# Kernel tuning notes

Measured on AMD Instinct MI355X. Metric: run time of the kernel, lower is better.

## Reference

```python
import jax, jax.numpy as jnp
import numpy as np

B, N, K, D, H, FF, L, NH = 8, 50, 20, 3, 128, 2048, 3, 8
S = N * K
HD = H // NH


def setup_inputs() -> dict:
    key = jax.random.key(0)
    ks = jax.random.split(key, 16)
    visited = jax.random.uniform(ks[0], (B, S)) < 0.05
    # the single most-recent action per batch row (status flips 0 -> 1)
    action_idx = jax.random.randint(ks[1], (B,), 0, S)
    visited = visited.at[jnp.arange(B), action_idx].set(True)
    feats = jax.random.normal(ks[2], (B, S, D - 1)) * visited[:, :, None]
    state = jnp.concatenate([feats, visited[:, :, None].astype(jnp.float32)], axis=-1)
    prev_state = state.at[jnp.arange(B), action_idx, :].set(0.0)

    def w(k, shape, s=0.02):
        return jax.random.normal(k, shape, dtype=jnp.float32) * s

    return dict(
        prev_state=prev_state, state=state,
        W_pre=w(ks[3], (D, H)), b_pre=jnp.zeros(H),
        Wq=w(ks[4], (L, H, H)), bq=jnp.zeros((L, H)),
        Wk=w(ks[5], (L, H, H)), bk=jnp.zeros((L, H)),
        Wv=w(ks[6], (L, H, H)), bv=jnp.zeros((L, H)),
        Wo=w(ks[7], (L, H, H)), bo=jnp.zeros((L, H)),
        ln1_g=jnp.ones((L, H)), ln1_b=jnp.zeros((L, H)),
        Wff1=w(ks[8], (L, H, FF)), bff1=jnp.zeros((L, FF)),
        Wff2=w(ks[9], (L, FF, H)), bff2=jnp.zeros((L, H)),
        ln2_g=jnp.ones((L, H)), ln2_b=jnp.zeros((L, H)),
        W_comb=w(ks[10], (2 * H, H)), b_comb=jnp.zeros(H),
        W_dec=w(ks[11], (H, H)), b_dec=jnp.zeros(H),
        W_lin=w(ks[12], (S, S)), b_lin=jnp.zeros(S),
    )


def _layer_norm(x, g, b, eps=1e-5):
    m = jnp.mean(x, -1, keepdims=True)
    v = jnp.mean(jnp.square(x - m), -1, keepdims=True)
    return (x - m) * jax.lax.rsqrt(v + eps) * g + b


def _update_mask(state):
    # vectorized equivalent of the original Python-loop scatter mask
    status = state[:, :, -1] != 0                      # visited [B, S], S = K*N channel-major
    mask = status
    vis_kn = status.reshape(B, K, N)
    user_any = vis_kn.any(axis=1)                      # [B, N]: user visited on any channel
    mask = mask | jnp.broadcast_to(user_any[:, None, :], (B, K, N)).reshape(B, S)
    assigned = state.reshape(B, K, N, D).sum(-1) != 0  # [B, K, N]
    full = assigned.sum(-1) >= 2                       # [B, K]: channel already has 2 users
    mask = mask | jnp.broadcast_to(full[:, :, None], (B, K, N)).reshape(B, S)
    return mask


def reference(prev_state, state, W_pre, b_pre, Wq, bq, Wk, bk, Wv, bv, Wo, bo,
              ln1_g, ln1_b, Wff1, bff1, Wff2, bff2, ln2_g, ln2_b,
              W_comb, b_comb, W_dec, b_dec, W_lin, b_lin):
    mask = _update_mask(state)
    # exactly one status change per batch row (sequential RL step)
    diff = prev_state[:, :, -1] != state[:, :, -1]
    act_idx = jnp.argmax(diff, axis=1)                 # [B]

    x = state @ W_pre + b_pre                          # [B, S, H]
    scale = np.float32(1.0 / np.sqrt(HD))
    for i in range(L):  # 3 post-LN transformer encoder layers
        q = (x @ Wq[i] + bq[i]).reshape(B, S, NH, HD)
        k = (x @ Wk[i] + bk[i]).reshape(B, S, NH, HD)
        v = (x @ Wv[i] + bv[i]).reshape(B, S, NH, HD)
        att = jax.nn.softmax(jnp.einsum('bqhd,bkhd->bhqk', q, k) * scale, axis=-1)
        o = jnp.einsum('bhqk,bkhd->bqhd', att, v).reshape(B, S, H) @ Wo[i] + bo[i]
        x = _layer_norm(x + o, ln1_g[i], ln1_b[i])
        ff = jax.nn.relu(x @ Wff1[i] + bff1[i]) @ Wff2[i] + bff2[i]
        x = _layer_norm(x + ff, ln2_g[i], ln2_b[i])

    last = x[jnp.arange(B), act_idx]                   # [B, H]
    combined = jnp.concatenate([x.mean(axis=1), last], axis=-1)  # [B, 2H]
    g = combined @ W_comb + b_comb                     # [B, H]
    dec = x @ W_dec + b_dec                            # [B, S, H]
    scores = jnp.einsum('bsh,bh->bs', dec, g)          # [B, S]
    masked = scores @ W_lin + b_lin                    # Q-Learning head
    return jnp.where(mask, -jnp.inf, masked)
```

## Files before the change

### kernel.cpp

```cpp
#include <hip/hip_runtime.h>
#include <math.h>

#define Bb 8
#define Ss 1000
#define Kk 20
#define Nn 50
#define Dd 3
#define Hh 128
#define FFf 2048
#define Ll 3
#define NHh 8
#define HDd 16
#define ROWS (Bb*Ss)

#define SENTINEL -3.0e38f

typedef unsigned short ush;
typedef short short8 __attribute__((ext_vector_type(8)));
typedef short short4v __attribute__((ext_vector_type(4)));
typedef float f32x4 __attribute__((ext_vector_type(4)));

__device__ __forceinline__ ush f2b(float f) {
  unsigned x = __float_as_uint(f);
  return (ush)((x + 0x7fff + ((x >> 16) & 1)) >> 16);
}

__global__ __launch_bounds__(256) void mask_kernel(const float* __restrict__ state,
                                                   const float* __restrict__ prev_state,
                                                   int* __restrict__ mask, int* __restrict__ act_idx) {
  int b = blockIdx.x, tid = threadIdx.x;
  __shared__ unsigned char status[Ss], assigned[Ss], uany[Nn], fullk[Kk];
  __shared__ int act;
  if (tid == 0) act = 1 << 30;
  __syncthreads();
  for (int s = tid; s < Ss; s += 256) {
    const float* st = state + ((size_t)b * Ss + s) * Dd;
    float f2 = st[2];
    status[s] = (f2 != 0.f);
    assigned[s] = ((st[0] + st[1] + f2) != 0.f);
    float p2 = prev_state[((size_t)b * Ss + s) * Dd + 2];
    if (p2 != f2) atomicMin(&act, s);
  }
  __syncthreads();
  if (tid < Nn) {
    unsigned char a = 0;
    for (int k = 0; k < Kk; ++k) a |= status[k * Nn + tid];
    uany[tid] = a;
  } else if (tid >= 64 && tid < 64 + Kk) {
    int k = tid - 64, cnt = 0;
    for (int n = 0; n < Nn; ++n) cnt += assigned[k * Nn + n];
    fullk[k] = (cnt >= 2);
  }
  __syncthreads();
  for (int s = tid; s < Ss; s += 256)
    mask[b * Ss + s] = (int)(status[s] | uany[s % Nn] | fullk[s / Nn]);
  if (tid == 0) act_idx[b] = (act >= Ss) ? 0 : act;
}

__global__ __launch_bounds__(256) void pre_kernel(const float* __restrict__ state,
                                                  const float* __restrict__ W_pre,
                                                  const float* __restrict__ b_pre,
                                                  float* __restrict__ x, ush* __restrict__ xbf,
                                                  float* __restrict__ mpart) {
  int idx = blockIdx.x * 256 + threadIdx.x;
  if (idx >= ROWS * Hh) return;
  if (idx < Bb * Hh) mpart[idx] = 0.f;
  int row = idx >> 7, n = idx & 127;
  const float* st = state + (size_t)row * Dd;
  float v = b_pre[n] + st[0] * W_pre[n] + st[1] * W_pre[Hh + n] + st[2] * W_pre[2 * Hh + n];
  x[idx] = v;
  xbf[idx] = f2b(v);
}

#define TQKV 144
#define TWO  48
#define TFF1 768
#define TFF2 768
#define TWD  16
#define TBIAS 5
#define TTOT (TQKV+TWO+TFF1+TFF2+TWD+TBIAS)
__global__ __launch_bounds__(256) void transpose_prep(
    const float* __restrict__ Wq, const float* __restrict__ Wk, const float* __restrict__ Wv,
    const float* __restrict__ Wo, const float* __restrict__ Wff1, const float* __restrict__ Wff2,
    const float* __restrict__ bq, const float* __restrict__ bk, const float* __restrict__ bv,
    const float* __restrict__ W_dec,
    ush* __restrict__ wqkvT, ush* __restrict__ woT, ush* __restrict__ wff1T, ush* __restrict__ wff2T,
    float* __restrict__ bqkv, float* __restrict__ wdecT) {
  int t = blockIdx.x, tid = threadIdx.x;
  if (t >= TTOT - TBIAS) {
    int idx = (t - (TTOT - TBIAS)) * 256 + tid;
    if (idx < Ll * 384) {
      int l = idx / 384, c = idx % 384;
      bqkv[idx] = (c < 128) ? bq[l * Hh + c] : (c < 256 ? bk[l * Hh + c - 128] : bv[l * Hh + c - 256]);
    }
    return;
  }
  __shared__ float lf[32][33];
  int tr = tid >> 5, tc = tid & 31;
  const float* s; ush* d = nullptr; float* df = nullptr;
  int sp, dp;
  if (t < TQKV) {
    int l = t / 48, rem = t % 48, mat = rem / 16, tt = rem % 16;
    int ti = tt >> 2, tj = tt & 3;
    const float* m = (mat == 0) ? Wq : (mat == 1) ? Wk : Wv;
    s = m + (size_t)l * 16384 + (size_t)(ti * 32) * 128 + tj * 32; sp = 128;
    d = wqkvT + ((size_t)l * 384 + mat * 128 + tj * 32) * 128 + ti * 32; dp = 128;
  } else if (t < TQKV + TWO) {
    int r0 = t - TQKV; int l = r0 / 16, tt = r0 % 16, ti = tt >> 2, tj = tt & 3;
    s = Wo + (size_t)l * 16384 + (size_t)(ti * 32) * 128 + tj * 32; sp = 128;
    d = woT + ((size_t)l * 128 + tj * 32) * 128 + ti * 32; dp = 128;
  } else if (t < TQKV + TWO + TFF1) {
    int r0 = t - TQKV - TWO; int l = r0 / 256, tt = r0 % 256, ti = tt >> 6, tj = tt & 63;
    s = Wff1 + (size_t)l * 128 * 2048 + (size_t)(ti * 32) * 2048 + tj * 32; sp = 2048;
    d = wff1T + ((size_t)l * 2048 + tj * 32) * 128 + ti * 32; dp = 128;
  } else if (t < TQKV + TWO + TFF1 + TFF2) {
    int r0 = t - TQKV - TWO - TFF1; int l = r0 / 256, tt = r0 % 256, ti = tt >> 2, tj = tt & 3;
    s = Wff2 + (size_t)l * 2048 * 128 + (size_t)(ti * 32) * 128 + tj * 32; sp = 128;
    d = wff2T + ((size_t)l * 128 + tj * 32) * 2048 + ti * 32; dp = 2048;
  } else {
    int tt = t - TQKV - TWO - TFF1 - TFF2; int ti = tt >> 2, tj = tt & 3;
    s = W_dec + (size_t)(ti * 32) * 128 + tj * 32; sp = 128;
    df = wdecT + (size_t)(tj * 32) * 128 + ti * 32; dp = 128;
  }
#pragma unroll
  for (int p = 0; p < 4; ++p) {
    int r = tr + p * 8;
    lf[r][tc] = s[(size_t)r * sp + tc];
  }
  __syncthreads();
#pragma unroll
  for (int p = 0; p < 4; ++p) {
    int r = tr + p * 8;
    if (d) d[(size_t)r * dp + tc] = f2b(lf[tc][r]);
    else   df[(size_t)r * dp + tc] = lf[tc][r];
  }
}

#define LDP 40
template <int RELU, int QKVV>
__global__ __launch_bounds__(256) void gemm_mfma(const ush* __restrict__ A, const ush* __restrict__ Wt,
                                                 const float* __restrict__ bias, ush* __restrict__ out,
                                                 int N, int K, ush* __restrict__ vTout) {
  __shared__ ush As[2][64 * LDP];
  __shared__ ush Bs[2][64 * LDP];
  int tid = threadIdx.x;
  int lane = tid & 63, wid = tid >> 6;
  int wr = wid >> 1, wc = wid & 1;
  int m0 = blockIdx.y * 64, n0 = blockIdx.x * 64;
  int lrow = tid >> 2, lk = (tid & 3) << 3;
  int quad = lane >> 4, l16 = lane & 15, kb = quad << 3;

  const ush* Ap = A + (size_t)(m0 + lrow) * K + lk;
  const ush* Bp = Wt + (size_t)(n0 + lrow) * K + lk;

  f32x4 acc[2][2];
#pragma unroll
  for (int i = 0; i < 2; ++i)
#pragma unroll
    for (int j = 0; j < 2; ++j) acc[i][j] = (f32x4){0.f, 0.f, 0.f, 0.f};

  short8 pa = *(const short8*)Ap;
  short8 pb = *(const short8*)Bp;
  *(short8*)&As[0][lrow * LDP + lk] = pa;
  *(short8*)&Bs[0][lrow * LDP + lk] = pb;
  __syncthreads();

  int NT = K >> 5;
  for (int it = 0; it < NT; ++it) {
    int cur = it & 1;
    bool have = (it + 1 < NT);
    if (have) {
      pa = *(const short8*)(Ap + (it + 1) * 32);
      pb = *(const short8*)(Bp + (it + 1) * 32);
    }
    short8 a0 = *(short8*)&As[cur][(wr * 32 + l16) * LDP + kb];
    short8 a1 = *(short8*)&As[cur][(wr * 32 + 16 + l16) * LDP + kb];
    short8 b0 = *(short8*)&Bs[cur][(wc * 32 + l16) * LDP + kb];
    short8 b1 = *(short8*)&Bs[cur][(wc * 32 + 16 + l16) * LDP + kb];
    acc[0][0] = __builtin_amdgcn_mfma_f32_16x16x32_bf16(a0, b0, acc[0][0], 0, 0, 0);
    acc[0][1] = __builtin_amdgcn_mfma_f32_16x16x32_bf16(a0, b1, acc[0][1], 0, 0, 0);
    acc[1][0] = __builtin_amdgcn_mfma_f32_16x16x32_bf16(a1, b0, acc[1][0], 0, 0, 0);
    acc[1][1] = __builtin_amdgcn_mfma_f32_16x16x32_bf16(a1, b1, acc[1][1], 0, 0, 0);
    if (have) {
      *(short8*)&As[cur ^ 1][lrow * LDP + lk] = pa;
      *(short8*)&Bs[cur ^ 1][lrow * LDP + lk] = pb;
    }
    __syncthreads();
  }

#pragma unroll
  for (int i = 0; i < 2; ++i)
#pragma unroll
    for (int j = 0; j < 2; ++j) {
      int col = n0 + wc * 32 + j * 16 + l16;
      int rbase = m0 + wr * 32 + i * 16 + quad * 4;
      float bval = bias[col];
      if (QKVV && col >= 256) {
        int bb2 = rbase / 1000, qq = rbase - bb2 * 1000;
        short4v pk;
#pragma unroll
        for (int v = 0; v < 4; ++v) pk[v] = (short)f2b(acc[i][j][v] + bval);
        *(short4v*)&vTout[((size_t)(bb2 * 128 + (col - 256))) * 1024 + qq] = pk;
      } else {
#pragma unroll
        for (int v = 0; v < 4; ++v) {
          float o = acc[i][j][v] + bval;
          if (RELU) o = fmaxf(o, 0.f);
          out[(size_t)(rbase + v) * N + col] = f2b(o);
        }
      }
    }
}

#define F2P 72
template <int MEANOUT>
__global__ __launch_bounds__(256) void gemm_ln_kernel(const ush* __restrict__ A,
                                                      const ush* __restrict__ Wt,
                                                      const float* __restrict__ bias,
                                                      const float* __restrict__ ln_g, const float* __restrict__ ln_b,
                                                      float* __restrict__ x, ush* __restrict__ xbf,
                                                      float* __restrict__ mpart) {
  const int KK = 2048;
  __shared__ ush As[2][32 * F2P];
  __shared__ ush Bs[2][128 * F2P];
  __shared__ float red1[2][2][16], red2[2][2][16];
  __shared__ float pbias[128], pg[128], pb[128];

  int tid = threadIdx.x, lane = tid & 63, w = tid >> 6;
  int wr = w & 1, wc = w >> 1;
  int l16 = lane & 15, quad = lane >> 4, kb = quad * 8;
  int m0 = blockIdx.x * 32;
  if (tid < 128) { pbias[tid] = bias[tid]; pg[tid] = ln_g[tid]; pb[tid] = ln_b[tid]; }

  f32x4 acc[4];
#pragma unroll
  for (int j = 0; j < 4; ++j) acc[j] = (f32x4){0.f, 0.f, 0.f, 0.f};

  int arow = tid >> 3, alk = (tid & 7) << 3;
  const ush* Ap = A + (size_t)(m0 + arow) * KK + alk;
  const ush* Bp = Wt + (size_t)arow * KK + alk;

  short8 pa = *(const short8*)Ap;
  short8 pbr[4];
#pragma unroll
  for (int rep = 0; rep < 4; ++rep)
    pbr[rep] = *(const short8*)(Bp + (size_t)rep * 32 * KK);
  *(short8*)&As[0][arow * F2P + alk] = pa;
#pragma unroll
  for (int rep = 0; rep < 4; ++rep)
    *(short8*)&Bs[0][(rep * 32 + arow) * F2P + alk] = pbr[rep];
  __syncthreads();

  const int NT = KK / 64;
  for (int it = 0; it < NT; ++it) {
    int cur = it & 1;
    bool have = (it + 1 < NT);
    if (have) {
      pa = *(const short8*)(Ap + (it + 1) * 64);
#pragma unroll
      for (int rep = 0; rep < 4; ++rep)
        pbr[rep] = *(const short8*)(Bp + (size_t)rep * 32 * KK + (it + 1) * 64);
    }
#pragma unroll
    for (int kk = 0; kk < 2; ++kk) {
      short8 a = *(short8*)&As[cur][(wr * 16 + l16) * F2P + kk * 32 + kb];
#pragma unroll
      for (int j = 0; j < 4; ++j) {
        short8 b = *(short8*)&Bs[cur][(wc * 64 + j * 16 + l16) * F2P + kk * 32 + kb];
        acc[j] = __builtin_amdgcn_mfma_f32_16x16x32_bf16(a, b, acc[j], 0, 0, 0);
      }
    }
    if (have) {
      *(short8*)&As[cur ^ 1][arow * F2P + alk] = pa;
#pragma unroll
      for (int rep = 0; rep < 4; ++rep)
        *(short8*)&Bs[cur ^ 1][(rep * 32 + arow) * F2P + alk] = pbr[rep];
    }
    __syncthreads();
  }

  float v[4][4], s1[4] = {0.f, 0.f, 0.f, 0.f}, s2[4] = {0.f, 0.f, 0.f, 0.f};
#pragma unroll
  for (int j = 0; j < 4; ++j) {
    int col = wc * 64 + j * 16 + l16;
#pragma unroll
    for (int r = 0; r < 4; ++r) {
      int row = m0 + wr * 16 + quad * 4 + r;
      float vv = acc[j][r] + pbias[col] + x[(size_t)row * Hh + col];
      v[j][r] = vv; s1[r] += vv; s2[r] += vv * vv;
    }
  }
#pragma unroll
  for (int m = 1; m <= 8; m <<= 1) {
#pragma unroll
    for (int r = 0; r < 4; ++r) { s1[r] += __shfl_xor(s1[r], m); s2[r] += __shfl_xor(s2[r], m); }
  }
  if (l16 == 0) {
#pragma unroll
    for (int r = 0; r < 4; ++r) {
      red1[wr][wc][quad * 4 + r] = s1[r];
      red2[wr][wc][quad * 4 + r] = s2[r];
    }
  }
  __syncthreads();
  float osum[4] = {0.f, 0.f, 0.f, 0.f};
#pragma unroll
  for (int r = 0; r < 4; ++r) {
    int qr = quad * 4 + r;
    float t1 = red1[wr][0][qr] + red1[wr][1][qr];
    float t2 = red2[wr][0][qr] + red2[wr][1][qr];
    float mean = t1 * (1.f / 128.f);
    float var = t2 * (1.f / 128.f) - mean * mean;
    float rstd = rsqrtf(var + 1e-5f);
    int row = m0 + wr * 16 + quad * 4 + r;
#pragma unroll
    for (int j = 0; j < 4; ++j) {
      int col = wc * 64 + j * 16 + l16;
      float o = (v[j][r] - mean) * rstd * pg[col] + pb[col];
      size_t gi = (size_t)row * Hh + col;
      x[gi] = o; xbf[gi] = f2b(o);
      if (MEANOUT) osum[j] += o;
    }
  }
  if (MEANOUT) {
    int gb = (m0 + wr * 16 + quad * 4) / 1000;
#pragma unroll
    for (int j = 0; j < 4; ++j)
      atomicAdd(&mpart[gb * 128 + wc * 64 + j * 16 + l16], osum[j]);
  }
}

__global__ __launch_bounds__(256) void gemm_ln16(const ush* __restrict__ A,
                                                 const ush* __restrict__ Wt,
                                                 const float* __restrict__ bias,
                                                 const float* __restrict__ ln_g, const float* __restrict__ ln_b,
                                                 float* __restrict__ x, ush* __restrict__ xbf) {
  __shared__ ush As[2][16 * F2P];
  __shared__ ush Bs[2][128 * F2P];
  __shared__ float red1[4][16], red2[4][16];
  __shared__ float pbias[128], pg[128], pb[128];

  int tid = threadIdx.x, lane = tid & 63, w = tid >> 6;
  int l16 = lane & 15, quad = lane >> 4, kb = quad * 8;
  int m0 = blockIdx.x * 16;
  if (tid < 128) { pbias[tid] = bias[tid]; pg[tid] = ln_g[tid]; pb[tid] = ln_b[tid]; }

  f32x4 acc[2];
  acc[0] = (f32x4){0.f, 0.f, 0.f, 0.f};
  acc[1] = (f32x4){0.f, 0.f, 0.f, 0.f};

  int srow = tid >> 3, slk = (tid & 7) << 3;
  const ush* Ap = A + (size_t)(m0 + srow) * 128 + slk;
  const ush* Bp = Wt + (size_t)srow * 128 + slk;

  short8 pa;
  short8 pbr[4];
  if (tid < 128) pa = *(const short8*)Ap;
#pragma unroll
  for (int rep = 0; rep < 4; ++rep)
    pbr[rep] = *(const short8*)(Bp + (size_t)rep * 32 * 128);
  if (tid < 128) *(short8*)&As[0][srow * F2P + slk] = pa;
#pragma unroll
  for (int rep = 0; rep < 4; ++rep)
    *(short8*)&Bs[0][(rep * 32 + srow) * F2P + slk] = pbr[rep];
  __syncthreads();

#pragma unroll
  for (int it = 0; it < 2; ++it) {
    if (it == 0) {
      if (tid < 128) pa = *(const short8*)(Ap + 64);
#pragma unroll
      for (int rep = 0; rep < 4; ++rep)
        pbr[rep] = *(const short8*)(Bp + (size_t)rep * 32 * 128 + 64);
    }
#pragma unroll
    for (int kk = 0; kk < 2; ++kk) {
      short8 a = *(short8*)&As[it][l16 * F2P + kk * 32 + kb];
#pragma unroll
      for (int j = 0; j < 2; ++j) {
        short8 b = *(short8*)&Bs[it][(w * 32 + j * 16 + l16) * F2P + kk * 32 + kb];
        acc[j] = __builtin_amdgcn_mfma_f32_16x16x32_bf16(a, b, acc[j], 0, 0, 0);
      }
    }
    if (it == 0) {
      if (tid < 128) *(short8*)&As[1][srow * F2P + slk] = pa;
#pragma unroll
      for (int rep = 0; rep < 4; ++rep)
        *(short8*)&Bs[1][(rep * 32 + srow) * F2P + slk] = pbr[rep];
    }
    __syncthreads();
  }

  float v[2][4], s1[4] = {0.f, 0.f, 0.f, 0.f}, s2[4] = {0.f, 0.f, 0.f, 0.f};
#pragma unroll
  for (int j = 0; j < 2; ++j) {
    int col = w * 32 + j * 16 + l16;
#pragma unroll
    for (int r = 0; r < 4; ++r) {
      int row = m0 + quad * 4 + r;
      float vv = acc[j][r] + pbias[col] + x[(size_t)row * Hh + col];
      v[j][r] = vv; s1[r] += vv; s2[r] += vv * vv;
    }
  }
#pragma unroll
  for (int m = 1; m <= 8; m <<= 1) {
#pragma unroll
    for (int r = 0; r < 4; ++r) { s1[r] += __shfl_xor(s1[r], m); s2[r] += __shfl_xor(s2[r], m); }
  }
  if (l16 == 0) {
#pragma unroll
    for (int r = 0; r < 4; ++r) {
      red1[w][quad * 4 + r] = s1[r];
      red2[w][quad * 4 + r] = s2[r];
    }
  }
  __syncthreads();
#pragma unroll
  for (int r = 0; r < 4; ++r) {
    int qr = quad * 4 + r;
    float t1 = red1[0][qr] + red1[1][qr] + red1[2][qr] + red1[3][qr];
    float t2 = red2[0][qr] + red2[1][qr] + red2[2][qr] + red2[3][qr];
    float mean = t1 * (1.f / 128.f);
    float var = t2 * (1.f / 128.f) - mean * mean;
    float rstd = rsqrtf(var + 1e-5f);
    int row = m0 + qr;
#pragma unroll
    for (int j = 0; j < 2; ++j) {
      int col = w * 32 + j * 16 + l16;
      float o = (v[j][r] - mean) * rstd * pg[col] + pb[col];
      size_t gi = (size_t)row * Hh + col;
      x[gi] = o; xbf[gi] = f2b(o);
    }
  }
}

__global__ __launch_bounds__(256) void attn_mfma(const ush* __restrict__ qkv,
                                                 const ush* __restrict__ vT,
                                                 ush* __restrict__ attn_o) {
  int blk = blockIdx.x;
  int local = blk >> 3;
  int bh = ((blk & 7) << 3) | (local >> 4);
  int qt = local & 15;
  int b = bh >> 3, h = bh & 7;
  int qbase = qt * 64;
  int tid = threadIdx.x, lane = tid & 63, w = tid >> 6;
  int l16 = lane & 15, quad = lane >> 4, kb = quad * 8;

  __shared__ ush Ks[2][64][40];
  __shared__ ush Vs[2][16][72];
  __shared__ ush Pb[4][16][72];

  if (tid < 128) {
    int row = tid >> 1, g = tid & 1;
    *(short8*)&Ks[0][row][16 + g * 8] = (short8){0, 0, 0, 0, 0, 0, 0, 0};
    *(short8*)&Ks[1][row][16 + g * 8] = (short8){0, 0, 0, 0, 0, 0, 0, 0};
  }

  int qrow = qbase + w * 16 + l16; if (qrow >= Ss) qrow = Ss - 1;
  short8 aq = *(const short8*)(qkv + (size_t)(b * Ss + qrow) * 384 + h * HDd + kb);

  int srow = tid >> 1, sg = tid & 1;
  int sd = (tid - 128) >> 3, skg = (tid - 128) & 7;
  const ush* kbase = qkv + (size_t)b * Ss * 384 + 128 + h * HDd;
  const ush* vbase = vT + (size_t)(b * 128 + h * 16) * 1024;

  if (tid < 128) {
    short8 s8 = (short8){0, 0, 0, 0, 0, 0, 0, 0};
    if (srow < Ss) s8 = *(const short8*)(kbase + (size_t)srow * 384 + sg * 8);
    *(short8*)&Ks[0][srow][sg * 8] = s8;
  } else {
    *(short8*)&Vs[0][sd][skg * 8] = *(const short8*)(vbase + (size_t)sd * 1024 + skg * 8);
  }
  __syncthreads();

  const short one_b = (short)0x3F80;
  const short8 ones = (short8){one_b, one_b, one_b, one_b, one_b, one_b, one_b, one_b};
  f32x4 acc_pv = (f32x4){0.f, 0.f, 0.f, 0.f};
  f32x4 acc_l = (f32x4){0.f, 0.f, 0.f, 0.f};
  const f32x4 zero4 = (f32x4){0.f, 0.f, 0.f, 0.f};

  for (int it = 0; it < 16; ++it) {
    int k0 = it * 64;
    int cur = it & 1, nxt = cur ^ 1;
    bool have = (it + 1 < 16);

    short8 gk, gv;
    if (have) {
      if (tid < 128) {
        gk = (short8){0, 0, 0, 0, 0, 0, 0, 0};
        int key = k0 + 64 + srow;
        if (key < Ss) gk = *(const short8*)(kbase + (size_t)key * 384 + sg * 8);
      } else {
        gv = *(const short8*)(vbase + (size_t)sd * 1024 + k0 + 64 + skg * 8);
      }
    }

    bool tail = (k0 + 64 > Ss);
#pragma unroll
    for (int kn = 0; kn < 4; ++kn) {
      short8 ak = *(short8*)&Ks[cur][kn * 16 + l16][kb];
      f32x4 s = __builtin_amdgcn_mfma_f32_16x16x32_bf16(ak, aq, zero4, 0, 0, 0);
      float p0 = __expf(s[0] * 0.25f);
      float p1 = __expf(s[1] * 0.25f);
      float p2 = __expf(s[2] * 0.25f);
      float p3 = __expf(s[3] * 0.25f);
      if (tail) {
        int keyb = k0 + kn * 16 + quad * 4;
        if (keyb + 0 >= Ss) p0 = 0.f;
        if (keyb + 1 >= Ss) p1 = 0.f;
        if (keyb + 2 >= Ss) p2 = 0.f;
        if (keyb + 3 >= Ss) p3 = 0.f;
      }
      unsigned lo, hi;
      asm("v_cvt_pk_bf16_f32 %0, %1, %2" : "=v"(lo) : "v"(p0), "v"(p1));
      asm("v_cvt_pk_bf16_f32 %0, %1, %2" : "=v"(hi) : "v"(p2), "v"(p3));
      *(uint2*)&Pb[w][l16][kn * 16 + quad * 4] = make_uint2(lo, hi);
    }

    short8 pa0 = *(short8*)&Pb[w][l16][kb];
    short8 pa1 = *(short8*)&Pb[w][l16][32 + kb];
    short8 vb0 = *(short8*)&Vs[cur][l16][kb];
    short8 vb1 = *(short8*)&Vs[cur][l16][32 + kb];
    acc_pv = __builtin_amdgcn_mfma_f32_16x16x32_bf16(pa0, vb0, acc_pv, 0, 0, 0);
    acc_pv = __builtin_amdgcn_mfma_f32_16x16x32_bf16(pa1, vb1, acc_pv, 0, 0, 0);
    acc_l = __builtin_amdgcn_mfma_f32_16x16x32_bf16(pa0, ones, acc_l, 0, 0, 0);
    acc_l = __builtin_amdgcn_mfma_f32_16x16x32_bf16(pa1, ones, acc_l, 0, 0, 0);

    if (have) {
      if (tid < 128) *(short8*)&Ks[nxt][srow][sg * 8] = gk;
      else *(short8*)&Vs[nxt][sd][skg * 8] = gv;
    }
    __syncthreads();
  }

#pragma unroll
  for (int r = 0; r < 4; ++r) {
    int q = qbase + w * 16 + quad * 4 + r;
    if (q < Ss)
      attn_o[((size_t)(b * Ss + q)) * Hh + h * HDd + l16] = f2b(acc_pv[r] / acc_l[r]);
  }
}

__global__ __launch_bounds__(128) void ghc_kernel(const float* __restrict__ x, const float* __restrict__ mpart,
                                                  const int* __restrict__ act_idx,
                                                  const float* __restrict__ W_comb, const float* __restrict__ b_comb,
                                                  const float* __restrict__ wdecT, const float* __restrict__ b_dec,
                                                  float* __restrict__ h, float* __restrict__ cb) {
  int b = blockIdx.x, n = threadIdx.x;
  __shared__ float cs[2 * Hh], gs[Hh], red[2];
  cs[n] = mpart[b * Hh + n] * (1.f / Ss);
  cs[Hh + n] = x[((size_t)b * Ss + act_idx[b]) * Hh + n];
  __syncthreads();
  float acc = b_comb[n];
  for (int j = 0; j < 2 * Hh; ++j) acc += cs[j] * W_comb[(size_t)j * Hh + n];
  gs[n] = acc;
  __syncthreads();
  float hv = 0.f;
  for (int c = 0; c < Hh; ++c) hv += wdecT[(size_t)c * Hh + n] * gs[c];
  h[b * Hh + n] = hv;
  float t = b_dec[n] * gs[n];
  for (int off = 32; off; off >>= 1) t += __shfl_down(t, off);
  if ((n & 63) == 0) red[n >> 6] = t;
  __syncthreads();
  if (n == 0) cb[b] = red[0] + red[1];
}

__global__ __launch_bounds__(256) void scores_kernel(const float* __restrict__ x, const float* __restrict__ h,
                                                     const float* __restrict__ cb, float* __restrict__ scores) {
  int wid = threadIdx.x >> 6, lane = threadIdx.x & 63;
  int row = blockIdx.x * 4 + wid;
  if (row >= ROWS) return;
  int b = row / Ss;
  const float* xr = x + (size_t)row * Hh;
  const float* hb = h + b * Hh;
  float s = xr[lane] * hb[lane] + xr[lane + 64] * hb[lane + 64];
  for (int off = 32; off; off >>= 1) s += __shfl_down(s, off);
  if (lane == 0) scores[row] = s + cb[b];
}

__global__ __launch_bounds__(256) void final_part(const float* __restrict__ scores,
                                                  const float* __restrict__ W_lin,
                                                  float* __restrict__ fpart) {
  int spc = blockIdx.x, kc = blockIdx.y;
  int tid = threadIdx.x;
  __shared__ float ss[8][125];
  for (int i = tid; i < 8 * 125; i += 256) {
    int bb = i / 125, s = i - bb * 125;
    ss[bb][s] = scores[bb * Ss + kc * 125 + s];
  }
  __syncthreads();
  if (tid < 250) {
    int sp = spc * 250 + tid;
    float acc[8];
#pragma unroll
    for (int bb = 0; bb < 8; ++bb) acc[bb] = 0.f;
    const float* wl = &W_lin[(size_t)(kc * 125) * Ss + sp];
#pragma unroll 5
    for (int s = 0; s < 125; ++s) {
      float wv = wl[(size_t)s * Ss];
#pragma unroll
      for (int bb = 0; bb < 8; ++bb) acc[bb] = fmaf(ss[bb][s], wv, acc[bb]);
    }
#pragma unroll
    for (int bb = 0; bb < 8; ++bb)
      fpart[((size_t)kc * Bb + bb) * Ss + sp] = acc[bb];
  }
}

__global__ __launch_bounds__(256) void final_combine(const float* __restrict__ fpart,
                                                     const float* __restrict__ b_lin,
                                                     const int* __restrict__ mask,
                                                     float* __restrict__ out) {
  int b = blockIdx.y;
  int sp = blockIdx.x * 256 + threadIdx.x;
  if (sp >= Ss) return;
  float acc = b_lin[sp];
#pragma unroll
  for (int kc = 0; kc < 8; ++kc) acc += fpart[((size_t)kc * Bb + b) * Ss + sp];
  out[b * Ss + sp] = mask[b * Ss + sp] ? SENTINEL : acc;
}

extern "C" void kernel_launch(void* const* d_in, const int* in_sizes, int n_in,
                              void* d_out, int out_size, void* d_ws, size_t ws_size,
                              hipStream_t stream) {
  const float* prev_state = (const float*)d_in[0];
  const float* state = (const float*)d_in[1];
  const float* W_pre = (const float*)d_in[2];
  const float* b_pre = (const float*)d_in[3];
  const float* Wq = (const float*)d_in[4];
  const float* bq = (const float*)d_in[5];
  const float* Wk = (const float*)d_in[6];
  const float* bk = (const float*)d_in[7];
  const float* Wv = (const float*)d_in[8];
  const float* bv = (const float*)d_in[9];
  const float* Wo = (const float*)d_in[10];
  const float* bo = (const float*)d_in[11];
  const float* ln1_g = (const float*)d_in[12];
  const float* ln1_b = (const float*)d_in[13];
  const float* Wff1 = (const float*)d_in[14];
  const float* bff1 = (const float*)d_in[15];
  const float* Wff2 = (const float*)d_in[16];
  const float* bff2 = (const float*)d_in[17];
  const float* ln2_g = (const float*)d_in[18];
  const float* ln2_b = (const float*)d_in[19];
  const float* W_comb = (const float*)d_in[20];
  const float* b_comb = (const float*)d_in[21];
  const float* W_dec = (const float*)d_in[22];
  const float* b_dec = (const float*)d_in[23];
  const float* W_lin = (const float*)d_in[24];
  const float* b_lin = (const float*)d_in[25];

  char* wsp = (char*)d_ws;
  auto alloc = [&](size_t bytes) { char* p = wsp; wsp += (bytes + 255) & ~(size_t)255; return p; };
  int* mask = (int*)alloc(ROWS * 4);
  int* act = (int*)alloc(Bb * 4);
  ush* wqkvT = (ush*)alloc((size_t)Ll * 384 * 128 * 2);
  ush* woT = (ush*)alloc((size_t)Ll * 128 * 128 * 2);
  ush* wff1T = (ush*)alloc((size_t)Ll * 2048 * 128 * 2);
  ush* wff2T = (ush*)alloc((size_t)Ll * 128 * 2048 * 2);
  float* bqkv = (float*)alloc((size_t)Ll * 384 * 4);
  float* wdecT = (float*)alloc((size_t)Hh * Hh * 4);
  float* x = (float*)alloc((size_t)ROWS * Hh * 4);
  ush* xbf = (ush*)alloc((size_t)ROWS * Hh * 2);
  ush* qkv_bf = (ush*)alloc((size_t)ROWS * 384 * 2);
  ush* vT = (ush*)alloc((size_t)Bb * 128 * 1024 * 2);
  ush* attn_ob = (ush*)alloc((size_t)ROWS * Hh * 2);
  float* mpart = (float*)alloc((size_t)Bb * Hh * 4);
  float* hbuf = (float*)alloc((size_t)Bb * Hh * 4);
  float* cb = (float*)alloc((size_t)Bb * 4);
  float* scores = (float*)alloc((size_t)ROWS * 4);
  float* fpart = (float*)alloc((size_t)8 * Bb * Ss * 4);
  ush* ffb = (ush*)alloc((size_t)ROWS * FFf * 2);

  transpose_prep<<<dim3(TTOT), 256, 0, stream>>>(Wq, Wk, Wv, Wo, Wff1, Wff2, bq, bk, bv, W_dec,
                                                 wqkvT, woT, wff1T, wff2T, bqkv, wdecT);
  mask_kernel<<<Bb, 256, 0, stream>>>(state, prev_state, mask, act);
  pre_kernel<<<dim3((ROWS * Hh + 255) / 256), 256, 0, stream>>>(state, W_pre, b_pre, x, xbf, mpart);

  for (int l = 0; l < Ll; ++l) {
    gemm_mfma<0, 1><<<dim3(384 / 64, ROWS / 64), 256, 0, stream>>>(
        xbf, wqkvT + (size_t)l * 384 * 128, bqkv + l * 384, qkv_bf, 384, 128, vT);
    attn_mfma<<<dim3(1024), 256, 0, stream>>>(qkv_bf, vT, attn_ob);
    gemm_ln16<<<dim3(ROWS / 16), 256, 0, stream>>>(
        attn_ob, woT + (size_t)l * 128 * 128, bo + l * Hh, ln1_g + l * Hh, ln1_b + l * Hh, x, xbf);
    gemm_mfma<1, 0><<<dim3(2048 / 64, ROWS / 64), 256, 0, stream>>>(
        xbf, wff1T + (size_t)l * 2048 * 128, bff1 + l * FFf, ffb, 2048, 128, nullptr);
    if (l == Ll - 1)
      gemm_ln_kernel<1><<<dim3(ROWS / 32), 256, 0, stream>>>(
          ffb, wff2T + (size_t)l * 128 * 2048, bff2 + l * Hh, ln2_g + l * Hh, ln2_b + l * Hh, x, xbf, mpart);
    else
      gemm_ln_kernel<0><<<dim3(ROWS / 32), 256, 0, stream>>>(
          ffb, wff2T + (size_t)l * 128 * 2048, bff2 + l * Hh, ln2_g + l * Hh, ln2_b + l * Hh, x, xbf, mpart);
  }

  ghc_kernel<<<Bb, 128, 0, stream>>>(x, mpart, act, W_comb, b_comb, wdecT, b_dec, hbuf, cb);
  scores_kernel<<<dim3(ROWS / 4), 256, 0, stream>>>(x, hbuf, cb, scores);
  final_part<<<dim3(4, 8), 256, 0, stream>>>(scores, W_lin, fpart);
  final_combine<<<dim3(4, Bb), 256, 0, stream>>>(fpart, b_lin, mask, (float*)d_out);
}
```

Measured before the change: 383.5 us.

## Use 512 threads in FF2+LayerNorm GEMM with manually unrolled double buffer

The FF2 GEMM fused with LayerNorm now runs 8 waves per block instead of 4, so each wave covers a 16x32 output slice rather than 16x64. B-tile loading is spread across 512 threads, and the K loop is unrolled by two with explicit ping-pong register prefetch. The aim is more waves in flight to hide latency and fewer accumulators per thread. In exchange there are more cross-wave LayerNorm reductions and the same number of barriers spread over more waves, with half of the threads idle during A loads.

```diff
diff --git a/kernel.cpp b/kernel.cpp
--- a/kernel.cpp
+++ b/kernel.cpp
@@ -214,7 +214,7 @@
 
 #define F2P 72
 template <int MEANOUT>
-__global__ __launch_bounds__(256) void gemm_ln_kernel(const ush* __restrict__ A,
+__global__ __launch_bounds__(512) void gemm_ln_kernel(const ush* __restrict__ A,
                                                       const ush* __restrict__ Wt,
                                                       const float* __restrict__ bias,
                                                       const float* __restrict__ ln_g, const float* __restrict__ ln_b,
@@ -223,7 +223,7 @@
   const int KK = 2048;
   __shared__ ush As[2][32 * F2P];
   __shared__ ush Bs[2][128 * F2P];
-  __shared__ float red1[2][2][16], red2[2][2][16];
+  __shared__ float red1[2][4][16], red2[2][4][16];
   __shared__ float pbias[128], pg[128], pb[128];
 
   int tid = threadIdx.x, lane = tid & 63, w = tid >> 6;
@@ -232,57 +232,74 @@
   int m0 = blockIdx.x * 32;
   if (tid < 128) { pbias[tid] = bias[tid]; pg[tid] = ln_g[tid]; pb[tid] = ln_b[tid]; }
 
-  f32x4 acc[4];
-#pragma unroll
-  for (int j = 0; j < 4; ++j) acc[j] = (f32x4){0.f, 0.f, 0.f, 0.f};
+  f32x4 acc[2];
+  acc[0] = (f32x4){0.f, 0.f, 0.f, 0.f};
+  acc[1] = (f32x4){0.f, 0.f, 0.f, 0.f};
 
   int arow = tid >> 3, alk = (tid & 7) << 3;
+  int brow = tid >> 2, bc = (tid & 3) << 4;
   const ush* Ap = A + (size_t)(m0 + arow) * KK + alk;
-  const ush* Bp = Wt + (size_t)arow * KK + alk;
-
-  short8 pa = *(const short8*)Ap;
-  short8 pbr[4];
-#pragma unroll
-  for (int rep = 0; rep < 4; ++rep)
-    pbr[rep] = *(const short8*)(Bp + (size_t)rep * 32 * KK);
-  *(short8*)&As[0][arow * F2P + alk] = pa;
-#pragma unroll
-  for (int rep = 0; rep < 4; ++rep)
-    *(short8*)&Bs[0][(rep * 32 + arow) * F2P + alk] = pbr[rep];
-  __syncthreads();
-
-  const int NT = KK / 64;
-  for (int it = 0; it < NT; ++it) {
-    int cur = it & 1;
-    bool have = (it + 1 < NT);
-    if (have) {
-      pa = *(const short8*)(Ap + (it + 1) * 64);
-#pragma unroll
-      for (int rep = 0; rep < 4; ++rep)
-        pbr[rep] = *(const short8*)(Bp + (size_t)rep * 32 * KK + (it + 1) * 64);
+  const ush* Bp = Wt + (size_t)brow * KK + bc;
+
+  short8 ra_a, rb_a, ra_b0, ra_b1, rb_b0, rb_b1;
+
+  if (tid < 256) ra_a = *(const short8*)Ap;
+  ra_b0 = *(const short8*)Bp;
+  ra_b1 = *(const short8*)(Bp + 8);
+  if (tid < 256) *(short8*)&As[0][arow * F2P + alk] = ra_a;
+  *(short8*)&Bs[0][brow * F2P + bc] = ra_b0;
+  *(short8*)&Bs[0][brow * F2P + bc + 8] = ra_b1;
+  if (tid < 256) rb_a = *(const short8*)(Ap + 64);
+  rb_b0 = *(const short8*)(Bp + 64);
+  rb_b1 = *(const short8*)(Bp + 64 + 8);
+  __syncthreads();
+
+  for (int k = 0; k < 16; ++k) {
+    int t2 = 2 * k + 2, t3 = 2 * k + 3;
+    if (t2 < 32) {
+      if (tid < 256) ra_a = *(const short8*)(Ap + t2 * 64);
+      ra_b0 = *(const short8*)(Bp + t2 * 64);
+      ra_b1 = *(const short8*)(Bp + t2 * 64 + 8);
     }
 #pragma unroll
     for (int kk = 0; kk < 2; ++kk) {
-      short8 a = *(short8*)&As[cur][(wr * 16 + l16) * F2P + kk * 32 + kb];
-#pragma unroll
-      for (int j = 0; j < 4; ++j) {
-        short8 b = *(short8*)&Bs[cur][(wc * 64 + j * 16 + l16) * F2P + kk * 32 + kb];
+      short8 a = *(short8*)&As[0][(wr * 16 + l16) * F2P + kk * 32 + kb];
+#pragma unroll
+      for (int j = 0; j < 2; ++j) {
+        short8 b = *(short8*)&Bs[0][(wc * 32 + j * 16 + l16) * F2P + kk * 32 + kb];
         acc[j] = __builtin_amdgcn_mfma_f32_16x16x32_bf16(a, b, acc[j], 0, 0, 0);
       }
     }
-    if (have) {
-      *(short8*)&As[cur ^ 1][arow * F2P + alk] = pa;
-#pragma unroll
-      for (int rep = 0; rep < 4; ++rep)
-        *(short8*)&Bs[cur ^ 1][(rep * 32 + arow) * F2P + alk] = pbr[rep];
-    }
+    if (tid < 256) *(short8*)&As[1][arow * F2P + alk] = rb_a;
+    *(short8*)&Bs[1][brow * F2P + bc] = rb_b0;
+    *(short8*)&Bs[1][brow * F2P + bc + 8] = rb_b1;
     __syncthreads();
-  }
-
-  float v[4][4], s1[4] = {0.f, 0.f, 0.f, 0.f}, s2[4] = {0.f, 0.f, 0.f, 0.f};
-#pragma unroll
-  for (int j = 0; j < 4; ++j) {
-    int col = wc * 64 + j * 16 + l16;
+    if (t3 < 32) {
+      if (tid < 256) rb_a = *(const short8*)(Ap + t3 * 64);
+      rb_b0 = *(const short8*)(Bp + t3 * 64);
+      rb_b1 = *(const short8*)(Bp + t3 * 64 + 8);
+    }
+#pragma unroll
+    for (int kk = 0; kk < 2; ++kk) {
+      short8 a = *(short8*)&As[1][(wr * 16 + l16) * F2P + kk * 32 + kb];
+#pragma unroll
+      for (int j = 0; j < 2; ++j) {
+        short8 b = *(short8*)&Bs[1][(wc * 32 + j * 16 + l16) * F2P + kk * 32 + kb];
+        acc[j] = __builtin_amdgcn_mfma_f32_16x16x32_bf16(a, b, acc[j], 0, 0, 0);
+      }
+    }
+    if (t2 < 32) {
+      if (tid < 256) *(short8*)&As[0][arow * F2P + alk] = ra_a;
+      *(short8*)&Bs[0][brow * F2P + bc] = ra_b0;
+      *(short8*)&Bs[0][brow * F2P + bc + 8] = ra_b1;
+    }
+    __syncthreads();
+  }
+
+  float v[2][4], s1[4] = {0.f, 0.f, 0.f, 0.f}, s2[4] = {0.f, 0.f, 0.f, 0.f};
+#pragma unroll
+  for (int j = 0; j < 2; ++j) {
+    int col = wc * 32 + j * 16 + l16;
 #pragma unroll
     for (int r = 0; r < 4; ++r) {
       int row = m0 + wr * 16 + quad * 4 + r;
@@ -303,19 +320,19 @@
     }
   }
   __syncthreads();
-  float osum[4] = {0.f, 0.f, 0.f, 0.f};
+  float osum[2] = {0.f, 0.f};
 #pragma unroll
   for (int r = 0; r < 4; ++r) {
     int qr = quad * 4 + r;
-    float t1 = red1[wr][0][qr] + red1[wr][1][qr];
-    float t2 = red2[wr][0][qr] + red2[wr][1][qr];
+    float t1 = red1[wr][0][qr] + red1[wr][1][qr] + red1[wr][2][qr] + red1[wr][3][qr];
+    float t2 = red2[wr][0][qr] + red2[wr][1][qr] + red2[wr][2][qr] + red2[wr][3][qr];
     float mean = t1 * (1.f / 128.f);
     float var = t2 * (1.f / 128.f) - mean * mean;
     float rstd = rsqrtf(var + 1e-5f);
-    int row = m0 + wr * 16 + quad * 4 + r;
-#pragma unroll
-    for (int j = 0; j < 4; ++j) {
-      int col = wc * 64 + j * 16 + l16;
+    int row = m0 + wr * 16 + qr;
+#pragma unroll
+    for (int j = 0; j < 2; ++j) {
+      int col = wc * 32 + j * 16 + l16;
       float o = (v[j][r] - mean) * rstd * pg[col] + pb[col];
       size_t gi = (size_t)row * Hh + col;
       x[gi] = o; xbf[gi] = f2b(o);
@@ -325,8 +342,8 @@
   if (MEANOUT) {
     int gb = (m0 + wr * 16 + quad * 4) / 1000;
 #pragma unroll
-    for (int j = 0; j < 4; ++j)
-      atomicAdd(&mpart[gb * 128 + wc * 64 + j * 16 + l16], osum[j]);
+    for (int j = 0; j < 2; ++j)
+      atomicAdd(&mpart[gb * 128 + wc * 32 + j * 16 + l16], osum[j]);
   }
 }
 
@@ -686,10 +703,10 @@
     gemm_mfma<1, 0><<<dim3(2048 / 64, ROWS / 64), 256, 0, stream>>>(
         xbf, wff1T + (size_t)l * 2048 * 128, bff1 + l * FFf, ffb, 2048, 128, nullptr);
     if (l == Ll - 1)
-      gemm_ln_kernel<1><<<dim3(ROWS / 32), 256, 0, stream>>>(
+      gemm_ln_kernel<1><<<dim3(ROWS / 32), 512, 0, stream>>>(
           ffb, wff2T + (size_t)l * 128 * 2048, bff2 + l * Hh, ln2_g + l * Hh, ln2_b + l * Hh, x, xbf, mpart);
     else
-      gemm_ln_kernel<0><<<dim3(ROWS / 32), 256, 0, stream>>>(
+      gemm_ln_kernel<0><<<dim3(ROWS / 32), 512, 0, stream>>>(
           ffb, wff2T + (size_t)l * 128 * 2048, bff2 + l * Hh, ln2_g + l * Hh, ln2_b + l * Hh, x, xbf, mpart);
   }
 
```

Result: faster. 363.6 us (-5.2%).
